# Performance work log

Measured on AMD Instinct MI355X. Metric: run time of the kernel, lower is better.

## Reference

```python
import jax, jax.numpy as jnp
import numpy as np

B, L, D, H, NLAYERS = 32, 2048, 1024, 16, 4
HD = D // H
NEG = -1e30


def setup_inputs() -> dict:
    key = jax.random.key(0)
    ks = jax.random.split(key, 12)
    tokens = jax.random.normal(ks[0], (B, L, D), dtype=jnp.float32)
    lengths = jax.random.randint(ks[1], (B,), 1, L + 1, dtype=jnp.int32)
    query_token = jax.random.normal(ks[2], (1, D), dtype=jnp.float32)
    s = 0.02
    Wq = jax.random.normal(ks[3], (NLAYERS, D, D), dtype=jnp.float32) * s
    Wk = jax.random.normal(ks[4], (NLAYERS, D, D), dtype=jnp.float32) * s
    Wv = jax.random.normal(ks[5], (NLAYERS, D, D), dtype=jnp.float32) * s
    Wo = jax.random.normal(ks[6], (NLAYERS, D, D), dtype=jnp.float32) * s
    bq = jnp.zeros((NLAYERS, D), jnp.float32)
    bk = jnp.zeros((NLAYERS, D), jnp.float32)
    bv = jnp.zeros((NLAYERS, D), jnp.float32)
    bo = jnp.zeros((NLAYERS, D), jnp.float32)
    gamma = jnp.ones((NLAYERS, D), jnp.float32)
    beta = jnp.zeros((NLAYERS, D), jnp.float32)
    return dict(tokens=tokens, lengths=lengths, query_token=query_token,
                Wq=Wq, bq=bq, Wk=Wk, bk=bk, Wv=Wv, bv=bv, Wo=Wo, bo=bo,
                gamma=gamma, beta=beta)


def _layernorm(x, g, b):
    mu = jnp.mean(x, axis=-1, keepdims=True)
    var = jnp.mean(jnp.square(x - mu), axis=-1, keepdims=True)
    return (x - mu) * jax.lax.rsqrt(var + 1e-5) * g + b


def reference(tokens, lengths, query_token, Wq, bq, Wk, bk, Wv, bv, Wo, bo, gamma, beta):
    # valid[b, l] = True where token l exists (inverse of key_padding_mask)
    valid = jnp.arange(L)[None, :] < lengths[:, None]            # [B, L]
    scale = 1.0 / jnp.sqrt(jnp.float32(HD))
    # zero out padded positions like the torch padded buffer (math-neutral)
    toks = tokens * valid[:, :, None].astype(tokens.dtype)       # [B, L, D]
    q = jnp.broadcast_to(query_token[None], (B, 1, D))           # [B, 1, D]
    for i in range(NLAYERS):
        qh = (q @ Wq[i] + bq[i]).reshape(B, 1, H, HD)            # [B, 1, H, hd]
        kh = (toks @ Wk[i] + bk[i]).reshape(B, L, H, HD)         # [B, L, H, hd]
        vh = (toks @ Wv[i] + bv[i]).reshape(B, L, H, HD)
        scores = jnp.einsum('bqhd,bkhd->bhqk', qh, kh) * scale   # [B, H, 1, L]
        scores = jnp.where(valid[:, None, None, :], scores, NEG)
        attn = jax.nn.softmax(scores, axis=-1)
        out = jnp.einsum('bhqk,bkhd->bqhd', attn, vh).reshape(B, 1, D)
        out = out @ Wo[i] + bo[i]
        q = _layernorm(out, gamma[i], beta[i])
    return q[:, 0, :]                                            # [B, D]
```

## Files before the change

kernel.cpp:

```cpp
#include <hip/hip_runtime.h>
#include <hip/hip_bf16.h>
#include <cstdint>
#include <cstddef>

#define BB 32
#define LL 2048
#define DD 1024
#define HH 16
#define HDIM 64
#define NL 4
#define NCHUNK 16
#define CHUNK 128
#define NEGINF -1e30f
#define PKS 16

typedef __attribute__((ext_vector_type(8))) short bf16x8;
typedef __attribute__((ext_vector_type(4))) float f32x4;

__device__ __forceinline__ unsigned short f2b(float x) {
    union { float f; unsigned int u; } v; v.f = x;
    unsigned int r = (v.u + 0x7FFFu + ((v.u >> 16) & 1u)) >> 16;
    return (unsigned short)r;
}
__device__ __forceinline__ float b2f(unsigned short u) {
    union { unsigned int u; float f; } v; v.u = ((unsigned int)u) << 16;
    return v.f;
}

template<int SRC>
__global__ __launch_bounds__(256) void k_gemv(
        const float* __restrict__ parts_in, const float* __restrict__ bias_in,
        const unsigned short* __restrict__ ctx16, const float* __restrict__ m_p,
        const float* __restrict__ s_p,
        const float* __restrict__ W, float* __restrict__ outp) {
    constexpr int KL = DD / PKS;
    int bid = blockIdx.x, tid = threadIdx.x;
    int ct = bid & 15, ks = bid >> 4;
    int e0 = ks * KL;
    __shared__ float Xs[BB][KL];
    __shared__ float wgtS[BB][NCHUNK];
    __shared__ float mgS[BB], SgS[BB];
    if (SRC == 3) {
        if (tid < BB) {
            int b = tid; float m = NEGINF;
            for (int c8 = 0; c8 < NCHUNK; ++c8)
                m = fmaxf(m, m_p[(b * NCHUNK + c8) * HH + ct]);
            float S = 0.f;
            for (int c8 = 0; c8 < NCHUNK; ++c8)
                S += s_p[(b * NCHUNK + c8) * HH + ct] *
                     __expf(m_p[(b * NCHUNK + c8) * HH + ct] - m);
            mgS[b] = m; SgS[b] = S;
        }
        __syncthreads();
#pragma unroll
        for (int j = 0; j < 2; ++j) {
            int idx = tid + j * 256;
            int b = idx >> 4, c8 = idx & 15;
            wgtS[b][c8] = __expf(m_p[(b * NCHUNK + c8) * HH + ct] - mgS[b]) / SgS[b];
        }
        __syncthreads();
    }
#pragma unroll
    for (int j = 0; j < 8; ++j) {
        int i = tid + j * 256;
        int b = i >> 6, k = i & 63;
        float x;
        if (SRC == 2) {
            x = bias_in[e0 + k];
#pragma unroll
            for (int j2 = 0; j2 < PKS; ++j2)
                x += parts_in[((size_t)(j2 * BB) + b) * DD + e0 + k];
        } else {
            x = 0.f;
#pragma unroll
            for (int c8 = 0; c8 < NCHUNK; ++c8)
                x += wgtS[b][c8] *
                     b2f(ctx16[(((size_t)(b * NCHUNK + c8)) * HH + ct) * DD + e0 + k]);
        }
        Xs[b][k] = x;
    }
    __syncthreads();
    int col = tid & 63, bg = tid >> 6;
    int c = ct * 64 + col;
    float acc[8] = {0.f, 0.f, 0.f, 0.f, 0.f, 0.f, 0.f, 0.f};
    for (int k = 0; k < KL; k += 4) {
        float w0 = W[(size_t)(e0 + k) * DD + c];
        float w1 = W[(size_t)(e0 + k + 1) * DD + c];
        float w2 = W[(size_t)(e0 + k + 2) * DD + c];
        float w3 = W[(size_t)(e0 + k + 3) * DD + c];
#pragma unroll
        for (int bb = 0; bb < 8; ++bb) {
            const float4 xv = *(const float4*)&Xs[bg * 8 + bb][k];
            acc[bb] += xv.x * w0 + xv.y * w1 + xv.z * w2 + xv.w * w3;
        }
    }
#pragma unroll
    for (int bb = 0; bb < 8; ++bb)
        outp[((size_t)(ks * BB) + bg * 8 + bb) * DD + c] = acc[bb];
}

__global__ __launch_bounds__(1024) void k_statsF(const float* __restrict__ parts,
        const float* __restrict__ bo, const float* __restrict__ gamma,
        const float* __restrict__ beta, float* __restrict__ outp) {
    int b = blockIdx.x, c = threadIdx.x;
    float v = bo[c];
#pragma unroll
    for (int ks = 0; ks < PKS; ++ks)
        v += parts[((size_t)(ks * BB) + b) * DD + c];
    float s1 = v, s2 = v * v;
#pragma unroll
    for (int off = 32; off; off >>= 1) {
        s1 += __shfl_xor(s1, off);
        s2 += __shfl_xor(s2, off);
    }
    __shared__ float r1[16], r2[16];
    __shared__ float smu, srs;
    int w = c >> 6;
    if ((c & 63) == 0) { r1[w] = s1; r2[w] = s2; }
    __syncthreads();
    if (c == 0) {
        float a = 0.f, q = 0.f;
#pragma unroll
        for (int i = 0; i < 16; ++i) { a += r1[i]; q += r2[i]; }
        float mu = a / (float)DD, var = q / (float)DD - mu * mu;
        smu = mu; srs = rsqrtf(var + 1e-5f);
    }
    __syncthreads();
    outp[(size_t)b * DD + c] = (v - smu) * srs * gamma[c] + beta[c];
}

__global__ __launch_bounds__(256) void k_qnext(const float* __restrict__ op,
        const float* __restrict__ bo, const float* __restrict__ gamma,
        const float* __restrict__ beta, const float* __restrict__ Wq,
        const float* __restrict__ bq, float* __restrict__ qh) {
    int bid = blockIdx.x, tid = threadIdx.x;
    int ct = bid & 15, bp = bid >> 4;
    int b0 = bp * 2;
    __shared__ float Xr[2][DD];
    __shared__ float pr[4][2][64];
    __shared__ float r1[4], r2[4];
    __shared__ float smu[2], srs[2];
#pragma unroll
    for (int j = 0; j < 8; ++j) {
        int idx = tid + j * 256;
        int bb = idx >> 10, c = idx & (DD - 1);
        float v = bo[c];
#pragma unroll
        for (int ks = 0; ks < PKS; ++ks)
            v += op[((size_t)(ks * BB) + b0 + bb) * DD + c];
        Xr[bb][c] = v;
    }
    __syncthreads();
    {
        int bb = tid >> 7, l = tid & 127;
        float s1 = 0.f, s2 = 0.f;
#pragma unroll
        for (int j = 0; j < 8; ++j) {
            float x = Xr[bb][l * 8 + j];
            s1 += x; s2 += x * x;
        }
#pragma unroll
        for (int off = 32; off; off >>= 1) {
            s1 += __shfl_xor(s1, off);
            s2 += __shfl_xor(s2, off);
        }
        int w = tid >> 6;
        if ((tid & 63) == 0) { r1[w] = s1; r2[w] = s2; }
    }
    __syncthreads();
    if (tid < 2) {
        float a = r1[tid * 2] + r1[tid * 2 + 1];
        float q = r2[tid * 2] + r2[tid * 2 + 1];
        float mu = a / (float)DD, var = q / (float)DD - mu * mu;
        smu[tid] = mu; srs[tid] = rsqrtf(var + 1e-5f);
    }
    __syncthreads();
    {
        int c = tid & 63, ks4 = tid >> 6;
        float mu0 = smu[0], rs0 = srs[0], mu1 = smu[1], rs1 = srs[1];
        float acc0 = 0.f, acc1 = 0.f;
        int k0 = ks4 * 256;
        for (int k = k0; k < k0 + 256; ++k) {
            float g = gamma[k], be = beta[k];
            float w = Wq[(size_t)k * DD + ct * 64 + c];
            float x0 = (Xr[0][k] - mu0) * rs0 * g + be;
            float x1 = (Xr[1][k] - mu1) * rs1 * g + be;
            acc0 += x0 * w;
            acc1 += x1 * w;
        }
        pr[ks4][0][c] = acc0;
        pr[ks4][1][c] = acc1;
    }
    __syncthreads();
    if (tid < 128) {
        int bb = tid >> 6, c = tid & 63;
        float q = bq[ct * 64 + c];
#pragma unroll
        for (int j = 0; j < 4; ++j) q += pr[j][bb][c];
        qh[((size_t)(b0 + bb)) * DD + ct * 64 + c] = q;
    }
}

__global__ __launch_bounds__(256) void k_q0(const float* __restrict__ qt,
        const float* __restrict__ Wq, const float* __restrict__ bq,
        float* __restrict__ qh) {
    int ct = blockIdx.x, tid = threadIdx.x;
    __shared__ float pr[4][64];
    int c = tid & 63, ks4 = tid >> 6;
    float acc = 0.f;
    int k0 = ks4 * 256;
    for (int k = k0; k < k0 + 256; ++k)
        acc += qt[k] * Wq[(size_t)k * DD + ct * 64 + c];
    pr[ks4][c] = acc;
    __syncthreads();
    if (tid < 64) {
        float q = bq[ct * 64 + tid];
#pragma unroll
        for (int j = 0; j < 4; ++j) q += pr[j][tid];
        qh[ct * 64 + tid] = q;
    }
}

template<int BCAST>
__global__ __launch_bounds__(256) void k_wk(const float* __restrict__ qh,
        const float* __restrict__ Wk, const float* __restrict__ bk,
        unsigned short* __restrict__ wk16, float* __restrict__ sb) {
    int h = blockIdx.x >> 4, et = blockIdx.x & 15;
    int tid = threadIdx.x;
    __shared__ float qs[BB][HDIM + 1];
    for (int i = tid; i < BB * HDIM; i += 256) {
        int bb = i >> 6, d = i & 63;
        qs[bb][d] = qh[((size_t)(BCAST ? 0 : bb)) * DD + h * HDIM + d];
    }
    __syncthreads();
    int b = tid & 31, eo = tid >> 5;
    for (int k = 0; k < 8; ++k) {
        int e = et * 64 + eo * 8 + k;
        const float* wrow = Wk + (size_t)e * DD + h * HDIM;
        float acc = 0.f;
#pragma unroll
        for (int d = 0; d < HDIM; ++d) acc += qs[b][d] * wrow[d];
        wk16[((size_t)(b * HH + h)) * DD + e] = f2b(acc);
    }
    if (et == 0 && tid < BB) {
        float acc = 0.f;
#pragma unroll
        for (int d = 0; d < HDIM; ++d) acc += qs[tid][d] * bk[h * HDIM + d];
        sb[tid * HH + h] = acc;
    }
}

template<int MODE>
__global__ __launch_bounds__(1024) void k_attn(const float* __restrict__ toks,
        unsigned short* __restrict__ tcache,
        const int* __restrict__ lens, const unsigned short* __restrict__ wk16,
        const float* __restrict__ sb, unsigned short* __restrict__ ctx16,
        float* __restrict__ m_p, float* __restrict__ s_p) {
    int b = blockIdx.x >> 4, chunk = blockIdx.x & 15;
    int tid = threadIdx.x, lane = tid & 63, w = tid >> 6;
    int len = lens[b];
    int base = chunk * CHUNK;
    int pidx = (b * NCHUNK + chunk) * HH;
    if (base >= len) {
        if (tid < HH) { m_p[pidx + tid] = NEGINF; s_p[pidx + tid] = 0.f; }
        return;
    }
    int nv = min(CHUNK, len - base);

    __shared__ __align__(16) unsigned short Tr[32][1032];
    __shared__ float Sred[16][HH][34];
    __shared__ unsigned short Pt[HH][40];
    __shared__ float sm_m[HH], sm_s[HH], sm_c[HH];

    if (tid < HH) { sm_m[tid] = NEGINF; sm_s[tid] = 0.f; }

    int hq = lane & 15, qg = lane >> 4;
    const unsigned short* wkb = wk16 + ((size_t)(b * HH + hq)) * DD + w * 64 + 8 * qg;
    bf16x8 afr0 = *(const bf16x8*)(wkb);
    bf16x8 afr1 = *(const bf16x8*)(wkb + 32);
    f32x4 zer = {0.f, 0.f, 0.f, 0.f};
    f32x4 ctxacc[4] = {zer, zer, zer, zer};
    float sbh = (tid < 512) ? sb[b * HH + (tid >> 5)] : 0.f;
    int st = tid >> 7;
    int se = (tid & 127) * 8;
    const size_t rowbase = (size_t)(b * LL + base);
    __syncthreads();

    for (int g = 0; g < CHUNK / 32; ++g) {
        int t0 = g * 32;
        if (t0 >= nv) break;
        if (MODE == 2) {
            const unsigned short* srcr = tcache + (rowbase + t0) * DD;
#pragma unroll
            for (int p = 0; p < 4; ++p) {
                int t = p * 8 + st;
                bf16x8 v = *(const bf16x8*)(srcr + (size_t)t * DD + se);
                *(bf16x8*)&Tr[t][se] = v;
            }
        } else {
            const float* srcr = toks + (rowbase + t0) * DD;
#pragma unroll
            for (int p = 0; p < 4; ++p) {
                int t = p * 8 + st;
                const float* sp = srcr + (size_t)t * DD + se;
                float4 a0 = *(const float4*)sp;
                float4 a1 = *(const float4*)(sp + 4);
                bf16x8 v;
                v[0] = f2b(a0.x); v[1] = f2b(a0.y); v[2] = f2b(a0.z); v[3] = f2b(a0.w);
                v[4] = f2b(a1.x); v[5] = f2b(a1.y); v[6] = f2b(a1.z); v[7] = f2b(a1.w);
                *(bf16x8*)&Tr[t][se] = v;
                if (MODE == 1)
                    *(bf16x8*)(tcache + (rowbase + t0 + t) * DD + se) = v;
            }
        }
        __syncthreads();
        f32x4 s0 = zer, s1 = zer;
        {
            int eb = w * 64 + 8 * qg;
            s0 = __builtin_amdgcn_mfma_f32_16x16x32_bf16(afr0, *(const bf16x8*)&Tr[hq][eb], s0, 0, 0, 0);
            s0 = __builtin_amdgcn_mfma_f32_16x16x32_bf16(afr1, *(const bf16x8*)&Tr[hq][eb + 32], s0, 0, 0, 0);
            s1 = __builtin_amdgcn_mfma_f32_16x16x32_bf16(afr0, *(const bf16x8*)&Tr[16 + hq][eb], s1, 0, 0, 0);
            s1 = __builtin_amdgcn_mfma_f32_16x16x32_bf16(afr1, *(const bf16x8*)&Tr[16 + hq][eb + 32], s1, 0, 0, 0);
        }
#pragma unroll
        for (int r = 0; r < 4; ++r) {
            Sred[w][qg * 4 + r][hq] = s0[r];
            Sred[w][qg * 4 + r][16 + hq] = s1[r];
        }
        __syncthreads();
        if (tid < 512) {
            int h = tid >> 5, t = tid & 31;
            float s = 0.f;
#pragma unroll
            for (int ww = 0; ww < 16; ++ww) s += Sred[ww][h][t];
            s = (s + sbh) * 0.125f;
            bool valid = (t0 + t) < nv;
            if (!valid) s = NEGINF;
            float tm = s;
#pragma unroll
            for (int off = 16; off; off >>= 1) tm = fmaxf(tm, __shfl_xor(tm, off, 32));
            float oldm = sm_m[h];
            float newm = fmaxf(oldm, tm);
            float pv = valid ? __expf(s - newm) : 0.f;
            float ps = pv;
#pragma unroll
            for (int off = 16; off; off >>= 1) ps += __shfl_xor(ps, off, 32);
            if (t == 0) {
                float corr = __expf(oldm - newm);
                sm_c[h] = corr;
                sm_m[h] = newm;
                sm_s[h] = sm_s[h] * corr + ps;
            }
            Pt[h][t] = f2b(pv);
        }
        __syncthreads();
        {
            float cr[4];
#pragma unroll
            for (int r = 0; r < 4; ++r) cr[r] = sm_c[qg * 4 + r];
            bf16x8 pafr;
            ushort4 pa0 = *(const ushort4*)&Pt[hq][8 * qg];
            ushort4 pa1 = *(const ushort4*)&Pt[hq][8 * qg + 4];
            pafr[0] = pa0.x; pafr[1] = pa0.y; pafr[2] = pa0.z; pafr[3] = pa0.w;
            pafr[4] = pa1.x; pafr[5] = pa1.y; pafr[6] = pa1.z; pafr[7] = pa1.w;
#pragma unroll
            for (int et = 0; et < 4; ++et) {
#pragma unroll
                for (int r = 0; r < 4; ++r) ctxacc[et][r] *= cr[r];
                bf16x8 bfr;
                int ec = w * 64 + et * 16 + hq;
#pragma unroll
                for (int i = 0; i < 8; ++i) bfr[i] = (short)Tr[8 * qg + i][ec];
                ctxacc[et] = __builtin_amdgcn_mfma_f32_16x16x32_bf16(pafr, bfr, ctxacc[et], 0, 0, 0);
            }
        }
        __syncthreads();
    }
    if (tid < HH) { m_p[pidx + tid] = sm_m[tid]; s_p[pidx + tid] = sm_s[tid]; }
#pragma unroll
    for (int et = 0; et < 4; ++et)
#pragma unroll
        for (int r = 0; r < 4; ++r) {
            int h = qg * 4 + r, e = w * 64 + et * 16 + hq;
            ctx16[((size_t)pidx + h) * DD + e] = f2b(ctxacc[et][r]);
        }
}

extern "C" void kernel_launch(void* const* d_in, const int* in_sizes, int n_in,
                              void* d_out, int out_size, void* d_ws, size_t ws_size,
                              hipStream_t stream) {
    const float* toks  = (const float*)d_in[0];
    const int*   lens  = (const int*)d_in[1];
    const float* qt    = (const float*)d_in[2];
    const float* Wq    = (const float*)d_in[3];
    const float* bq    = (const float*)d_in[4];
    const float* Wk    = (const float*)d_in[5];
    const float* bk    = (const float*)d_in[6];
    const float* Wv    = (const float*)d_in[7];
    const float* bv    = (const float*)d_in[8];
    const float* Wo    = (const float*)d_in[9];
    const float* bo    = (const float*)d_in[10];
    const float* gamma = (const float*)d_in[11];
    const float* beta  = (const float*)d_in[12];
    float* out = (float*)d_out;
    float* ws  = (float*)d_ws;

    unsigned short* ctx16 = (unsigned short*)ws;
    float* m_p   = ws + 4194304;
    float* s_p   = ws + 4202496;
    float* pvp   = ws + 4210688;
    float* op    = ws + 4734976;
    float* qh    = ws + 5259264;
    float* sbuf  = ws + 5292032;
    unsigned short* wk16 = (unsigned short*)(ws + 5292544);
    const size_t base_floats = 5554688;
    unsigned short* tcache = (unsigned short*)(ws + base_floats);
    const size_t need_cache = base_floats * 4 + (size_t)BB * LL * DD * 2;
    const bool use_cache = (ws_size >= need_cache);

    k_q0<<<16, 256, 0, stream>>>(qt, Wq, bq, qh);
    k_wk<1><<<256, 256, 0, stream>>>(qh, Wk, bk, wk16, sbuf);

    for (int i = 0; i < NL; ++i) {
        if (use_cache) {
            if (i == 0)
                k_attn<1><<<512, 1024, 0, stream>>>(toks, tcache, lens, wk16,
                        sbuf, ctx16, m_p, s_p);
            else
                k_attn<2><<<512, 1024, 0, stream>>>(toks, tcache, lens, wk16,
                        sbuf, ctx16, m_p, s_p);
        } else {
            k_attn<0><<<512, 1024, 0, stream>>>(toks, tcache, lens, wk16,
                    sbuf, ctx16, m_p, s_p);
        }
        const float* Wv_i = Wv + (size_t)i * DD * DD;
        const float* Wo_i = Wo + (size_t)i * DD * DD;
        k_gemv<3><<<256, 256, 0, stream>>>(nullptr, nullptr, ctx16, m_p, s_p,
                Wv_i, pvp);
        k_gemv<2><<<256, 256, 0, stream>>>(pvp, bv + i * DD, nullptr, nullptr,
                nullptr, Wo_i, op);
        if (i == NL - 1) {
            k_statsF<<<32, 1024, 0, stream>>>(op, bo + i * DD, gamma + i * DD,
                    beta + i * DD, out);
        } else {
            k_qnext<<<256, 256, 0, stream>>>(op, bo + i * DD, gamma + i * DD,
                    beta + i * DD, Wq + (size_t)(i + 1) * DD * DD,
                    bq + (i + 1) * DD, qh);
            k_wk<0><<<256, 256, 0, stream>>>(qh, Wk + (size_t)(i + 1) * DD * DD,
                    bk + (i + 1) * DD, wk16, sbuf);
        }
    }
}
```

Before: 394.2 us.

## Halve attention chunk count and widen gemv/qnext blocks to 512 threads

Attention chunks double from 128 to 256 tokens, halving the attention grid and the partial softmax/context buffers that the Wv gemv must reduce. The gemv and qnext kernels move to 512 threads per block with float4-vectorized input reduction and fewer rows per thread, which raises parallelism in the small GEMV stages. The trade-off is fewer attention blocks (256 on a large GPU) and longer per-block loops over tokens, which can hurt load balance across the variable sequence lengths.

```diff
diff --git a/kernel.cpp b/kernel.cpp
--- a/kernel.cpp
+++ b/kernel.cpp
@@ -9,8 +9,8 @@
 #define HH 16
 #define HDIM 64
 #define NL 4
-#define NCHUNK 16
-#define CHUNK 128
+#define NCHUNK 8
+#define CHUNK 256
 #define NEGINF -1e30f
 #define PKS 16
 
@@ -28,7 +28,7 @@
 }
 
 template<int SRC>
-__global__ __launch_bounds__(256) void k_gemv(
+__global__ __launch_bounds__(512) void k_gemv(
         const float* __restrict__ parts_in, const float* __restrict__ bias_in,
         const unsigned short* __restrict__ ctx16, const float* __restrict__ m_p,
         const float* __restrict__ s_p,
@@ -52,51 +52,55 @@
             mgS[b] = m; SgS[b] = S;
         }
         __syncthreads();
-#pragma unroll
-        for (int j = 0; j < 2; ++j) {
-            int idx = tid + j * 256;
-            int b = idx >> 4, c8 = idx & 15;
+        if (tid < 256) {
+            int b = tid >> 3, c8 = tid & 7;
             wgtS[b][c8] = __expf(m_p[(b * NCHUNK + c8) * HH + ct] - mgS[b]) / SgS[b];
         }
         __syncthreads();
     }
-#pragma unroll
-    for (int j = 0; j < 8; ++j) {
-        int i = tid + j * 256;
-        int b = i >> 6, k = i & 63;
-        float x;
+    {
+        int b = tid >> 4, kq = tid & 15;
+        int k = kq * 4;
+        float x0, x1, x2, x3;
         if (SRC == 2) {
-            x = bias_in[e0 + k];
-#pragma unroll
-            for (int j2 = 0; j2 < PKS; ++j2)
-                x += parts_in[((size_t)(j2 * BB) + b) * DD + e0 + k];
+            const float4 bi = *(const float4*)&bias_in[e0 + k];
+            x0 = bi.x; x1 = bi.y; x2 = bi.z; x3 = bi.w;
+#pragma unroll
+            for (int j2 = 0; j2 < PKS; ++j2) {
+                const float4 v = *(const float4*)&parts_in[((size_t)(j2 * BB) + b) * DD + e0 + k];
+                x0 += v.x; x1 += v.y; x2 += v.z; x3 += v.w;
+            }
         } else {
-            x = 0.f;
-#pragma unroll
-            for (int c8 = 0; c8 < NCHUNK; ++c8)
-                x += wgtS[b][c8] *
-                     b2f(ctx16[(((size_t)(b * NCHUNK + c8)) * HH + ct) * DD + e0 + k]);
-        }
-        Xs[b][k] = x;
+            x0 = x1 = x2 = x3 = 0.f;
+#pragma unroll
+            for (int c8 = 0; c8 < NCHUNK; ++c8) {
+                const ushort4 u = *(const ushort4*)&ctx16[(((size_t)(b * NCHUNK + c8)) * HH + ct) * DD + e0 + k];
+                float wq = wgtS[b][c8];
+                x0 += wq * b2f(u.x); x1 += wq * b2f(u.y);
+                x2 += wq * b2f(u.z); x3 += wq * b2f(u.w);
+            }
+        }
+        float4 xv = {x0, x1, x2, x3};
+        *(float4*)&Xs[b][k] = xv;
     }
     __syncthreads();
     int col = tid & 63, bg = tid >> 6;
     int c = ct * 64 + col;
-    float acc[8] = {0.f, 0.f, 0.f, 0.f, 0.f, 0.f, 0.f, 0.f};
+    float acc[4] = {0.f, 0.f, 0.f, 0.f};
     for (int k = 0; k < KL; k += 4) {
         float w0 = W[(size_t)(e0 + k) * DD + c];
         float w1 = W[(size_t)(e0 + k + 1) * DD + c];
         float w2 = W[(size_t)(e0 + k + 2) * DD + c];
         float w3 = W[(size_t)(e0 + k + 3) * DD + c];
 #pragma unroll
-        for (int bb = 0; bb < 8; ++bb) {
-            const float4 xv = *(const float4*)&Xs[bg * 8 + bb][k];
+        for (int bb = 0; bb < 4; ++bb) {
+            const float4 xv = *(const float4*)&Xs[bg * 4 + bb][k];
             acc[bb] += xv.x * w0 + xv.y * w1 + xv.z * w2 + xv.w * w3;
         }
     }
 #pragma unroll
-    for (int bb = 0; bb < 8; ++bb)
-        outp[((size_t)(ks * BB) + bg * 8 + bb) * DD + c] = acc[bb];
+    for (int bb = 0; bb < 4; ++bb)
+        outp[((size_t)(ks * BB) + bg * 4 + bb) * DD + c] = acc[bb];
 }
 
 __global__ __launch_bounds__(1024) void k_statsF(const float* __restrict__ parts,
@@ -129,7 +133,7 @@
     outp[(size_t)b * DD + c] = (v - smu) * srs * gamma[c] + beta[c];
 }
 
-__global__ __launch_bounds__(256) void k_qnext(const float* __restrict__ op,
+__global__ __launch_bounds__(512) void k_qnext(const float* __restrict__ op,
         const float* __restrict__ bo, const float* __restrict__ gamma,
         const float* __restrict__ beta, const float* __restrict__ Wq,
         const float* __restrict__ bq, float* __restrict__ qh) {
@@ -137,28 +141,26 @@
     int ct = bid & 15, bp = bid >> 4;
     int b0 = bp * 2;
     __shared__ float Xr[2][DD];
-    __shared__ float pr[4][2][64];
-    __shared__ float r1[4], r2[4];
+    __shared__ float pr[8][2][64];
+    __shared__ float r1[8], r2[8];
     __shared__ float smu[2], srs[2];
-#pragma unroll
-    for (int j = 0; j < 8; ++j) {
-        int idx = tid + j * 256;
-        int bb = idx >> 10, c = idx & (DD - 1);
-        float v = bo[c];
-#pragma unroll
-        for (int ks = 0; ks < PKS; ++ks)
-            v += op[((size_t)(ks * BB) + b0 + bb) * DD + c];
-        Xr[bb][c] = v;
-    }
-    __syncthreads();
     {
-        int bb = tid >> 7, l = tid & 127;
-        float s1 = 0.f, s2 = 0.f;
-#pragma unroll
-        for (int j = 0; j < 8; ++j) {
-            float x = Xr[bb][l * 8 + j];
-            s1 += x; s2 += x * x;
-        }
+        int bb = tid >> 8, c4 = tid & 255;
+        int c = c4 * 4;
+        float4 x = *(const float4*)&bo[c];
+#pragma unroll
+        for (int ks = 0; ks < PKS; ++ks) {
+            const float4 v = *(const float4*)&op[((size_t)(ks * BB) + b0 + bb) * DD + c];
+            x.x += v.x; x.y += v.y; x.z += v.z; x.w += v.w;
+        }
+        *(float4*)&Xr[bb][c] = x;
+    }
+    __syncthreads();
+    {
+        int bb = tid >> 8, l = tid & 255;
+        const float4 x = *(const float4*)&Xr[bb][l * 4];
+        float s1 = x.x + x.y + x.z + x.w;
+        float s2 = x.x * x.x + x.y * x.y + x.z * x.z + x.w * x.w;
 #pragma unroll
         for (int off = 32; off; off >>= 1) {
             s1 += __shfl_xor(s1, off);
@@ -169,18 +171,18 @@
     }
     __syncthreads();
     if (tid < 2) {
-        float a = r1[tid * 2] + r1[tid * 2 + 1];
-        float q = r2[tid * 2] + r2[tid * 2 + 1];
+        float a = r1[tid * 4] + r1[tid * 4 + 1] + r1[tid * 4 + 2] + r1[tid * 4 + 3];
+        float q = r2[tid * 4] + r2[tid * 4 + 1] + r2[tid * 4 + 2] + r2[tid * 4 + 3];
         float mu = a / (float)DD, var = q / (float)DD - mu * mu;
         smu[tid] = mu; srs[tid] = rsqrtf(var + 1e-5f);
     }
     __syncthreads();
     {
-        int c = tid & 63, ks4 = tid >> 6;
+        int c = tid & 63, ks8 = tid >> 6;
         float mu0 = smu[0], rs0 = srs[0], mu1 = smu[1], rs1 = srs[1];
         float acc0 = 0.f, acc1 = 0.f;
-        int k0 = ks4 * 256;
-        for (int k = k0; k < k0 + 256; ++k) {
+        int k0 = ks8 * 128;
+        for (int k = k0; k < k0 + 128; ++k) {
             float g = gamma[k], be = beta[k];
             float w = Wq[(size_t)k * DD + ct * 64 + c];
             float x0 = (Xr[0][k] - mu0) * rs0 * g + be;
@@ -188,15 +190,15 @@
             acc0 += x0 * w;
             acc1 += x1 * w;
         }
-        pr[ks4][0][c] = acc0;
-        pr[ks4][1][c] = acc1;
+        pr[ks8][0][c] = acc0;
+        pr[ks8][1][c] = acc1;
     }
     __syncthreads();
     if (tid < 128) {
         int bb = tid >> 6, c = tid & 63;
         float q = bq[ct * 64 + c];
 #pragma unroll
-        for (int j = 0; j < 4; ++j) q += pr[j][bb][c];
+        for (int j = 0; j < 8; ++j) q += pr[j][bb][c];
         qh[((size_t)(b0 + bb)) * DD + ct * 64 + c] = q;
     }
 }
@@ -256,7 +258,7 @@
         const int* __restrict__ lens, const unsigned short* __restrict__ wk16,
         const float* __restrict__ sb, unsigned short* __restrict__ ctx16,
         float* __restrict__ m_p, float* __restrict__ s_p) {
-    int b = blockIdx.x >> 4, chunk = blockIdx.x & 15;
+    int b = blockIdx.x >> 3, chunk = blockIdx.x & 7;
     int tid = threadIdx.x, lane = tid & 63, w = tid >> 6;
     int len = lens[b];
     int base = chunk * CHUNK;
@@ -286,7 +288,7 @@
     const size_t rowbase = (size_t)(b * LL + base);
     __syncthreads();
 
-    for (int g = 0; g < CHUNK / 32; ++g) {
+    for (int g = 0; g < 8; ++g) {
         int t0 = g * 32;
         if (t0 >= nv) break;
         if (MODE == 2) {
@@ -406,14 +408,14 @@
     float* ws  = (float*)d_ws;
 
     unsigned short* ctx16 = (unsigned short*)ws;
-    float* m_p   = ws + 4194304;
-    float* s_p   = ws + 4202496;
-    float* pvp   = ws + 4210688;
-    float* op    = ws + 4734976;
-    float* qh    = ws + 5259264;
-    float* sbuf  = ws + 5292032;
-    unsigned short* wk16 = (unsigned short*)(ws + 5292544);
-    const size_t base_floats = 5554688;
+    float* m_p   = ws + 2097152;
+    float* s_p   = ws + 2101248;
+    float* pvp   = ws + 2105344;
+    float* op    = ws + 2629632;
+    float* qh    = ws + 3153920;
+    float* sbuf  = ws + 3186688;
+    unsigned short* wk16 = (unsigned short*)(ws + 3187200);
+    const size_t base_floats = 3449344;
     unsigned short* tcache = (unsigned short*)(ws + base_floats);
     const size_t need_cache = base_floats * 4 + (size_t)BB * LL * DD * 2;
     const bool use_cache = (ws_size >= need_cache);
@@ -424,26 +426,26 @@
     for (int i = 0; i < NL; ++i) {
         if (use_cache) {
             if (i == 0)
-                k_attn<1><<<512, 1024, 0, stream>>>(toks, tcache, lens, wk16,
+                k_attn<1><<<256, 1024, 0, stream>>>(toks, tcache, lens, wk16,
                         sbuf, ctx16, m_p, s_p);
             else
-                k_attn<2><<<512, 1024, 0, stream>>>(toks, tcache, lens, wk16,
+                k_attn<2><<<256, 1024, 0, stream>>>(toks, tcache, lens, wk16,
                         sbuf, ctx16, m_p, s_p);
         } else {
-            k_attn<0><<<512, 1024, 0, stream>>>(toks, tcache, lens, wk16,
+            k_attn<0><<<256, 1024, 0, stream>>>(toks, tcache, lens, wk16,
                     sbuf, ctx16, m_p, s_p);
         }
         const float* Wv_i = Wv + (size_t)i * DD * DD;
         const float* Wo_i = Wo + (size_t)i * DD * DD;
-        k_gemv<3><<<256, 256, 0, stream>>>(nullptr, nullptr, ctx16, m_p, s_p,
+        k_gemv<3><<<256, 512, 0, stream>>>(nullptr, nullptr, ctx16, m_p, s_p,
                 Wv_i, pvp);
-        k_gemv<2><<<256, 256, 0, stream>>>(pvp, bv + i * DD, nullptr, nullptr,
+        k_gemv<2><<<256, 512, 0, stream>>>(pvp, bv + i * DD, nullptr, nullptr,
                 nullptr, Wo_i, op);
         if (i == NL - 1) {
             k_statsF<<<32, 1024, 0, stream>>>(op, bo + i * DD, gamma + i * DD,
                     beta + i * DD, out);
         } else {
-            k_qnext<<<256, 256, 0, stream>>>(op, bo + i * DD, gamma + i * DD,
+            k_qnext<<<256, 512, 0, stream>>>(op, bo + i * DD, gamma + i * DD,
                     beta + i * DD, Wq + (size_t)(i + 1) * DD * DD,
                     bq + (i + 1) * DD, qh);
             k_wk<0><<<256, 256, 0, stream>>>(qh, Wk + (size_t)(i + 1) * DD * DD,
```

Result: faster. 338.5 us (-14.1%).
